# Optimization experiments

Hardware: AMD Instinct MI355X
Metric: run time of the kernel (lower is better)

The kernel has to match this reference:

```python
import jax, jax.numpy as jnp
import numpy as np
import math

BLOCK = 32
TAU = 0.1
INIT_SPARSITY = 0.1


def setup_inputs() -> dict:
    key = jax.random.key(0)
    k1, k2, k3, k4 = jax.random.split(key, 4)
    B, S, D_IN, D_OUT = 4, 2048, 4096, 4096
    x = jax.random.normal(k1, (B, S, D_IN), dtype=jnp.float32)
    # nn.Linear default init: uniform(-1/sqrt(in), 1/sqrt(in))
    bound = 1.0 / math.sqrt(D_IN)
    weight = jax.random.uniform(k2, (D_OUT, D_IN), minval=-bound, maxval=bound, dtype=jnp.float32)
    bias = jax.random.uniform(k3, (D_OUT,), minval=-bound, maxval=bound, dtype=jnp.float32)
    # scores init per _init_scores: randn*0.1 + logit(init_sparsity)
    target_logit = math.log(INIT_SPARSITY / (1.0 - INIT_SPARSITY))
    scores = jax.random.normal(k4, (D_OUT // BLOCK, D_IN // BLOCK), dtype=jnp.float32) * 0.1 + target_logit
    return {"x": x, "weight": weight, "bias": bias, "scores": scores}


def reference(x, weight, bias, scores):
    # block mask: sigmoid(scores) > tau, expanded 32x32 per block
    block_mask = (jax.nn.sigmoid(scores) > TAU).astype(weight.dtype)  # [O/32, I/32]
    full_mask = jnp.repeat(jnp.repeat(block_mask, BLOCK, axis=0), BLOCK, axis=1)  # [O, I]
    pruned_weight = weight * full_mask
    # F.linear: x @ W^T + b
    return jnp.einsum('bsi,oi->bso', x, pruned_weight) + bias
```

## Files before the change

### kernel.cpp

```cpp
#include <hip/hip_runtime.h>


#define BM 128
#define BN 128
#define BK 32

typedef __attribute__((ext_vector_type(8))) short bf16x8;
typedef __attribute__((ext_vector_type(4))) float f32x4;

__device__ __forceinline__ unsigned short f2bf(float f) {
    union { float f; unsigned u; } v; v.f = f;
    return (unsigned short)((v.u + 0x7FFFu + ((v.u >> 16) & 1u)) >> 16);
}

#define THRESH (-2.1972245773362196f)


__global__ void conv_x(const float* __restrict__ X, unsigned short* __restrict__ Xb) {
    const long i = ((long)blockIdx.x * 256 + threadIdx.x) * 8;
    const float4 a = *(const float4*)(X + i);
    const float4 b = *(const float4*)(X + i + 4);
    ushort4 p, q;
    p.x = f2bf(a.x); p.y = f2bf(a.y); p.z = f2bf(a.z); p.w = f2bf(a.w);
    q.x = f2bf(b.x); q.y = f2bf(b.y); q.z = f2bf(b.z); q.w = f2bf(b.w);
    *(ushort4*)(Xb + i) = p;
    *(ushort4*)(Xb + i + 4) = q;
}

__global__ void conv_w(const float* __restrict__ W, const float* __restrict__ scores,
                       unsigned short* __restrict__ Wb, int K, int KB) {
    const long i = ((long)blockIdx.x * 256 + threadIdx.x) * 8;
    const int n = (int)(i / K);
    const int k = (int)(i % K);
    const float msk = (scores[(n >> 5) * KB + (k >> 5)] > THRESH) ? 1.0f : 0.0f;
    const float4 a = *(const float4*)(W + i);
    const float4 b = *(const float4*)(W + i + 4);
    ushort4 p, q;
    p.x = f2bf(a.x * msk); p.y = f2bf(a.y * msk); p.z = f2bf(a.z * msk); p.w = f2bf(a.w * msk);
    q.x = f2bf(b.x * msk); q.y = f2bf(b.y * msk); q.z = f2bf(b.z * msk); q.w = f2bf(b.w * msk);
    *(ushort4*)(Wb + i) = p;
    *(ushort4*)(Wb + i + 4) = q;
}

__global__ void pack_mask(const float* __restrict__ scores, unsigned long long* __restrict__ mb,
                          int KB) {
    const int nb = blockIdx.x;
    const int l  = threadIdx.x;
    const unsigned long long b0 = __ballot(scores[nb * KB + l] > THRESH);
    const unsigned long long b1 = __ballot(scores[nb * KB + 64 + l] > THRESH);
    if (l == 0) { mb[nb * 2] = b0; mb[nb * 2 + 1] = b1; }
}


__device__ __forceinline__ unsigned long long rfl64(unsigned long long v) {
    unsigned lo = __builtin_amdgcn_readfirstlane((unsigned)v);
    unsigned hi = __builtin_amdgcn_readfirstlane((unsigned)(v >> 32));
    return ((unsigned long long)hi << 32) | lo;
}

#define GLL16(g, l) __builtin_amdgcn_global_load_lds( \
    (const __attribute__((address_space(1))) void*)(g), \
    (__attribute__((address_space(3))) void*)(l), 16, 0, 0)

__global__ __launch_bounds__(256)
void mpl_main(const unsigned short* __restrict__ Xb,
              const unsigned short* __restrict__ Wb,
              const float* __restrict__ bias,
              const unsigned long long* __restrict__ mb,
              float* __restrict__ out, int M, int N, int K)
{
    __shared__ unsigned short sA[BM * BK];
    __shared__ unsigned short sB[BN * BK];

    const int tid  = threadIdx.x;
    const int lane = tid & 63;
    const int wave = tid >> 6;
    const int m0   = blockIdx.y * BM;
    const int n0   = blockIdx.x * BN;
    const int wm   = (wave & 1) * 64;
    const int wn   = (wave >> 1) * 64;
    const int KB   = K >> 5;

    const int nbb  = n0 >> 5;
    const int mynb = nbb + (wn >> 5);
    const unsigned long long w0lo = rfl64(mb[mynb * 2]),       w0hi = rfl64(mb[mynb * 2 + 1]);
    const unsigned long long w1lo = rfl64(mb[(mynb + 1) * 2]), w1hi = rfl64(mb[(mynb + 1) * 2 + 1]);
    const unsigned long long anylo = rfl64(mb[nbb*2] | mb[nbb*2+2] | mb[nbb*2+4] | mb[nbb*2+6]);
    const unsigned long long anyhi = rfl64(mb[nbb*2+1] | mb[nbb*2+3] | mb[nbb*2+5] | mb[nbb*2+7]);

    f32x4 acc[4][4];
#pragma unroll
    for (int i = 0; i < 4; i++)
#pragma unroll
        for (int j = 0; j < 4; j++)
            acc[i][j] = (f32x4){0.f, 0.f, 0.f, 0.f};

    const int srow = tid >> 2;
    const int scol = (tid & 3) * 16;
    const char* gA0 = (const char*)Xb + (long)(m0 + srow) * K * 2 + scol;
    const char* gA1 = (const char*)Xb + (long)(m0 + srow + 64) * K * 2 + scol;
    const char* gB0 = (const char*)Wb + (long)(n0 + srow) * K * 2 + scol;
    const char* gB1 = (const char*)Wb + (long)(n0 + srow + 64) * K * 2 + scol;
    char* sAc = (char*)sA;
    char* sBc = (char*)sB;
    char* ldsA0 = sAc + wave * 1024;
    char* ldsA1 = sAc + wave * 1024 + 4096;
    char* ldsB0 = sBc + wave * 1024;
    char* ldsB1 = sBc + wave * 1024 + 4096;

    const int fr = lane & 15;
    const int kq = (lane >> 4) * 8;

    for (int kb = 0; kb < KB; kb++) {
        const bool any = (kb < 64) ? ((anylo >> kb) & 1ULL) : ((anyhi >> (kb - 64)) & 1ULL);
        if (!any) continue;

        const long ko = (long)kb * 64;
        GLL16(gA0 + ko, ldsA0);
        GLL16(gA1 + ko, ldsA1);
        GLL16(gB0 + ko, ldsB0);
        GLL16(gB1 + ko, ldsB1);
        __syncthreads();

        bf16x8 af[4];
#pragma unroll
        for (int mi = 0; mi < 4; mi++)
            af[mi] = *(const bf16x8*)&sA[(wm + mi * 16 + fr) * BK + kq];

        const bool b0 = (kb < 64) ? ((w0lo >> kb) & 1ULL) : ((w0hi >> (kb - 64)) & 1ULL);
        const bool b1 = (kb < 64) ? ((w1lo >> kb) & 1ULL) : ((w1hi >> (kb - 64)) & 1ULL);

        if (b0) {
            bf16x8 bf0 = *(const bf16x8*)&sB[(wn + 0 * 16 + fr) * BK + kq];
            bf16x8 bf1 = *(const bf16x8*)&sB[(wn + 1 * 16 + fr) * BK + kq];
#pragma unroll
            for (int mi = 0; mi < 4; mi++) {
                acc[mi][0] = __builtin_amdgcn_mfma_f32_16x16x32_bf16(af[mi], bf0, acc[mi][0], 0, 0, 0);
                acc[mi][1] = __builtin_amdgcn_mfma_f32_16x16x32_bf16(af[mi], bf1, acc[mi][1], 0, 0, 0);
            }
        }
        if (b1) {
            bf16x8 bf2 = *(const bf16x8*)&sB[(wn + 2 * 16 + fr) * BK + kq];
            bf16x8 bf3 = *(const bf16x8*)&sB[(wn + 3 * 16 + fr) * BK + kq];
#pragma unroll
            for (int mi = 0; mi < 4; mi++) {
                acc[mi][2] = __builtin_amdgcn_mfma_f32_16x16x32_bf16(af[mi], bf2, acc[mi][2], 0, 0, 0);
                acc[mi][3] = __builtin_amdgcn_mfma_f32_16x16x32_bf16(af[mi], bf3, acc[mi][3], 0, 0, 0);
            }
        }
        __syncthreads();
    }

    const int cn = lane & 15;
    const int rq = (lane >> 4) * 4;
#pragma unroll
    for (int ni = 0; ni < 4; ni++) {
        const int n = n0 + wn + ni * 16 + cn;
        const float b = bias[n];
#pragma unroll
        for (int mi = 0; mi < 4; mi++) {
#pragma unroll
            for (int r = 0; r < 4; r++) {
                const int m = m0 + wm + mi * 16 + rq + r;
                out[(long)m * N + n] = acc[mi][ni][r] + b;
            }
        }
    }
}


#define LDSS (BK + 8)
__global__ __launch_bounds__(256, 2)
void mpl_gemm_fb(const float* __restrict__ X, const float* __restrict__ W,
                 const float* __restrict__ bias, const float* __restrict__ scores,
                 float* __restrict__ out, int M, int N, int K)
{
    __shared__ unsigned short sA[BM * LDSS];
    __shared__ unsigned short sB[BN * LDSS];
    const int tid = threadIdx.x;
    const int m0 = blockIdx.y * BM, n0 = blockIdx.x * BN;
    const int wave = tid >> 6, lane = tid & 63;
    const int wm = (wave & 1) * 64, wn = (wave >> 1) * 64;
    const int kblocks = K >> 5;
    f32x4 acc[4][4];
#pragma unroll
    for (int i = 0; i < 4; i++)
#pragma unroll
        for (int j = 0; j < 4; j++) acc[i][j] = (f32x4){0.f,0.f,0.f,0.f};
    int srow[4], sc4[4], snb[4];
#pragma unroll
    for (int i = 0; i < 4; i++) {
        int f = tid + 256 * i;
        srow[i] = f >> 3; sc4[i] = f & 7; snb[i] = (n0 + srow[i]) >> 5;
    }
    for (int k0 = 0; k0 < K; k0 += BK) {
        const int kb = k0 >> 5;
#pragma unroll
        for (int i = 0; i < 4; i++) {
            const float4 v = *(const float4*)(X + (long)(m0 + srow[i]) * K + k0 + sc4[i] * 4);
            ushort4 p; p.x = f2bf(v.x); p.y = f2bf(v.y); p.z = f2bf(v.z); p.w = f2bf(v.w);
            *(ushort4*)&sA[srow[i] * LDSS + sc4[i] * 4] = p;
        }
#pragma unroll
        for (int i = 0; i < 4; i++) {
            const float msk = (scores[snb[i] * kblocks + kb] > THRESH) ? 1.0f : 0.0f;
            const float4 v = *(const float4*)(W + (long)(n0 + srow[i]) * K + k0 + sc4[i] * 4);
            ushort4 p; p.x = f2bf(v.x*msk); p.y = f2bf(v.y*msk); p.z = f2bf(v.z*msk); p.w = f2bf(v.w*msk);
            *(ushort4*)&sB[srow[i] * LDSS + sc4[i] * 4] = p;
        }
        __syncthreads();
        const int fr = lane & 15, kq = (lane >> 4) * 8;
        bf16x8 af[4], bfr[4];
#pragma unroll
        for (int mi = 0; mi < 4; mi++) af[mi] = *(const bf16x8*)&sA[(wm + mi*16 + fr) * LDSS + kq];
#pragma unroll
        for (int ni = 0; ni < 4; ni++) bfr[ni] = *(const bf16x8*)&sB[(wn + ni*16 + fr) * LDSS + kq];
#pragma unroll
        for (int mi = 0; mi < 4; mi++)
#pragma unroll
            for (int ni = 0; ni < 4; ni++)
                acc[mi][ni] = __builtin_amdgcn_mfma_f32_16x16x32_bf16(af[mi], bfr[ni], acc[mi][ni], 0,0,0);
        __syncthreads();
    }
    const int cn = lane & 15, rq = (lane >> 4) * 4;
#pragma unroll
    for (int ni = 0; ni < 4; ni++) {
        const int n = n0 + wn + ni * 16 + cn;
        const float b = bias[n];
#pragma unroll
        for (int mi = 0; mi < 4; mi++)
#pragma unroll
            for (int r = 0; r < 4; r++)
                out[(long)(m0 + wm + mi*16 + rq + r) * N + n] = acc[mi][ni][r] + b;
    }
}

extern "C" void kernel_launch(void* const* d_in, const int* in_sizes, int n_in,
                              void* d_out, int out_size, void* d_ws, size_t ws_size,
                              hipStream_t stream) {
    const float* X      = (const float*)d_in[0];
    const float* W      = (const float*)d_in[1];
    const float* bias   = (const float*)d_in[2];
    const float* scores = (const float*)d_in[3];
    float* out          = (float*)d_out;

    const int N = in_sizes[2];
    const int K = in_sizes[1] / N;
    const int M = in_sizes[0] / K;
    const int KB = K >> 5;
    const int NB = N >> 5;

    const size_t mk2 = (size_t)M * K * 2;
    const size_t nk2 = (size_t)N * K * 2;
    const size_t need = mk2 + nk2 + (size_t)NB * 16;

    if (ws_size >= need && KB == 128 && (M % 128) == 0 && (N % 128) == 0 && (K % 2048) == 0) {
        unsigned short* Xb = (unsigned short*)d_ws;
        unsigned short* Wb = (unsigned short*)((char*)d_ws + mk2);
        unsigned long long* mbits = (unsigned long long*)((char*)d_ws + mk2 + nk2);

        conv_x<<<(int)((long)M * K / 2048), 256, 0, stream>>>(X, Xb);
        conv_w<<<(int)((long)N * K / 2048), 256, 0, stream>>>(W, scores, Wb, K, KB);
        pack_mask<<<NB, 64, 0, stream>>>(scores, mbits, KB);

        dim3 grid(N / BN, M / BM);
        mpl_main<<<grid, dim3(256), 0, stream>>>(Xb, Wb, bias, mbits, out, M, N, K);
    } else {
        dim3 grid(N / BN, M / BM);
        mpl_gemm_fb<<<grid, dim3(256), 0, stream>>>(X, W, bias, scores, out, M, N, K);
    }
}
```

Measured before the change: 546.8 us.

## Double K tile to 64 with XOR-swizzled LDS and fuse prep kernels

Merges the three preprocessing kernels (X conversion, masked W conversion, mask bit packing) into one launch. It also doubles the main GEMM's K tile to 64 with an XOR-swizzled LDS layout to avoid bank conflicts. B loads are now skipped per 32-row block when that block's mask bits are zero. The larger tile halves the number of barriers per K and cuts launch overhead, at the cost of coarser skipping, since a 64-wide step loads if either 32-block is active.

New measurement: 477.6 us. 1.14x faster.

```diff
diff --git a/kernel.cpp b/kernel.cpp
--- a/kernel.cpp
+++ b/kernel.cpp
@@ -3,7 +3,7 @@
 
 #define BM 128
 #define BN 128
-#define BK 32
+#define BK 64
 
 typedef __attribute__((ext_vector_type(8))) short bf16x8;
 typedef __attribute__((ext_vector_type(4))) float f32x4;
@@ -15,40 +15,47 @@
 
 #define THRESH (-2.1972245773362196f)
 
-
-__global__ void conv_x(const float* __restrict__ X, unsigned short* __restrict__ Xb) {
-    const long i = ((long)blockIdx.x * 256 + threadIdx.x) * 8;
-    const float4 a = *(const float4*)(X + i);
-    const float4 b = *(const float4*)(X + i + 4);
-    ushort4 p, q;
-    p.x = f2bf(a.x); p.y = f2bf(a.y); p.z = f2bf(a.z); p.w = f2bf(a.w);
-    q.x = f2bf(b.x); q.y = f2bf(b.y); q.z = f2bf(b.z); q.w = f2bf(b.w);
-    *(ushort4*)(Xb + i) = p;
-    *(ushort4*)(Xb + i + 4) = q;
-}
-
-__global__ void conv_w(const float* __restrict__ W, const float* __restrict__ scores,
-                       unsigned short* __restrict__ Wb, int K, int KB) {
-    const long i = ((long)blockIdx.x * 256 + threadIdx.x) * 8;
-    const int n = (int)(i / K);
-    const int k = (int)(i % K);
-    const float msk = (scores[(n >> 5) * KB + (k >> 5)] > THRESH) ? 1.0f : 0.0f;
-    const float4 a = *(const float4*)(W + i);
-    const float4 b = *(const float4*)(W + i + 4);
-    ushort4 p, q;
-    p.x = f2bf(a.x * msk); p.y = f2bf(a.y * msk); p.z = f2bf(a.z * msk); p.w = f2bf(a.w * msk);
-    q.x = f2bf(b.x * msk); q.y = f2bf(b.y * msk); q.z = f2bf(b.z * msk); q.w = f2bf(b.w * msk);
-    *(ushort4*)(Wb + i) = p;
-    *(ushort4*)(Wb + i + 4) = q;
-}
-
-__global__ void pack_mask(const float* __restrict__ scores, unsigned long long* __restrict__ mb,
-                          int KB) {
-    const int nb = blockIdx.x;
-    const int l  = threadIdx.x;
-    const unsigned long long b0 = __ballot(scores[nb * KB + l] > THRESH);
-    const unsigned long long b1 = __ballot(scores[nb * KB + 64 + l] > THRESH);
-    if (l == 0) { mb[nb * 2] = b0; mb[nb * 2 + 1] = b1; }
+__global__ void prep(const float* __restrict__ X, const float* __restrict__ W,
+                     const float* __restrict__ scores,
+                     unsigned short* __restrict__ Xb, unsigned short* __restrict__ Wb,
+                     unsigned long long* __restrict__ mbits,
+                     int M, int N, int K) {
+    const int b   = blockIdx.x;
+    const int tid = threadIdx.x;
+    const int KBlk = K >> 5;
+
+    if (b < M + N) {
+        const float* src;
+        unsigned short* dst;
+        const bool isW = (b >= M);
+        const int n = isW ? (b - M) : 0;
+        if (isW) { src = W + (long)n * K; dst = Wb + (long)n * K; }
+        else     { src = X + (long)b * K; dst = Xb + (long)b * K; }
+        const float* srow = isW ? scores + (long)(n >> 5) * KBlk : nullptr;
+
+        for (int k = tid * 16; k < K; k += 4096) {
+            const float msk = isW ? ((srow[k >> 5] > THRESH) ? 1.0f : 0.0f) : 1.0f;
+            const float4 a = *(const float4*)(src + k);
+            const float4 c = *(const float4*)(src + k + 4);
+            const float4 e = *(const float4*)(src + k + 8);
+            const float4 g = *(const float4*)(src + k + 12);
+            ushort4 p, q, r, s;
+            p.x = f2bf(a.x * msk); p.y = f2bf(a.y * msk); p.z = f2bf(a.z * msk); p.w = f2bf(a.w * msk);
+            q.x = f2bf(c.x * msk); q.y = f2bf(c.y * msk); q.z = f2bf(c.z * msk); q.w = f2bf(c.w * msk);
+            r.x = f2bf(e.x * msk); r.y = f2bf(e.y * msk); r.z = f2bf(e.z * msk); r.w = f2bf(e.w * msk);
+            s.x = f2bf(g.x * msk); s.y = f2bf(g.y * msk); s.z = f2bf(g.z * msk); s.w = f2bf(g.w * msk);
+            *(ushort4*)(dst + k)      = p;
+            *(ushort4*)(dst + k + 4)  = q;
+            *(ushort4*)(dst + k + 8)  = r;
+            *(ushort4*)(dst + k + 12) = s;
+        }
+    } else {
+        const int nb = (b - (M + N)) * 4 + (tid >> 6);
+        const int l  = tid & 63;
+        const unsigned long long b0 = __ballot(scores[(long)nb * KBlk + l] > THRESH);
+        const unsigned long long b1 = __ballot(scores[(long)nb * KBlk + 64 + l] > THRESH);
+        if (l == 0) { mbits[nb * 2] = b0; mbits[nb * 2 + 1] = b1; }
+    }
 }
 
 
@@ -79,14 +86,15 @@
     const int n0   = blockIdx.x * BN;
     const int wm   = (wave & 1) * 64;
     const int wn   = (wave >> 1) * 64;
-    const int KB   = K >> 5;
-
-    const int nbb  = n0 >> 5;
-    const int mynb = nbb + (wn >> 5);
-    const unsigned long long w0lo = rfl64(mb[mynb * 2]),       w0hi = rfl64(mb[mynb * 2 + 1]);
-    const unsigned long long w1lo = rfl64(mb[(mynb + 1) * 2]), w1hi = rfl64(mb[(mynb + 1) * 2 + 1]);
-    const unsigned long long anylo = rfl64(mb[nbb*2] | mb[nbb*2+2] | mb[nbb*2+4] | mb[nbb*2+6]);
-    const unsigned long long anyhi = rfl64(mb[nbb*2+1] | mb[nbb*2+3] | mb[nbb*2+5] | mb[nbb*2+7]);
+    const long K2  = (long)K * 2;
+
+    const int nbb = n0 >> 5;
+    unsigned long long mlo[4], mhi[4];
+#pragma unroll
+    for (int i = 0; i < 4; i++) {
+        mlo[i] = rfl64(mb[(nbb + i) * 2]);
+        mhi[i] = rfl64(mb[(nbb + i) * 2 + 1]);
+    }
 
     f32x4 acc[4][4];
 #pragma unroll
@@ -95,60 +103,77 @@
         for (int j = 0; j < 4; j++)
             acc[i][j] = (f32x4){0.f, 0.f, 0.f, 0.f};
 
-    const int srow = tid >> 2;
-    const int scol = (tid & 3) * 16;
-    const char* gA0 = (const char*)Xb + (long)(m0 + srow) * K * 2 + scol;
-    const char* gA1 = (const char*)Xb + (long)(m0 + srow + 64) * K * 2 + scol;
-    const char* gB0 = (const char*)Wb + (long)(n0 + srow) * K * 2 + scol;
-    const char* gB1 = (const char*)Wb + (long)(n0 + srow + 64) * K * 2 + scol;
+    const int r8   = tid >> 3;
+    const int cswz = ((tid & 7) ^ ((tid >> 3) & 7)) * 16;
+    const char* gA = (const char*)Xb + (long)(m0 + r8) * K2 + cswz;
+    const char* gB = (const char*)Wb + (long)(n0 + r8) * K2 + cswz;
     char* sAc = (char*)sA;
     char* sBc = (char*)sB;
-    char* ldsA0 = sAc + wave * 1024;
-    char* ldsA1 = sAc + wave * 1024 + 4096;
-    char* ldsB0 = sBc + wave * 1024;
-    char* ldsB1 = sBc + wave * 1024 + 4096;
-
-    const int fr = lane & 15;
-    const int kq = (lane >> 4) * 8;
-
-    for (int kb = 0; kb < KB; kb++) {
-        const bool any = (kb < 64) ? ((anylo >> kb) & 1ULL) : ((anyhi >> (kb - 64)) & 1ULL);
-        if (!any) continue;
-
-        const long ko = (long)kb * 64;
-        GLL16(gA0 + ko, ldsA0);
-        GLL16(gA1 + ko, ldsA1);
-        GLL16(gB0 + ko, ldsB0);
-        GLL16(gB1 + ko, ldsB1);
-        __syncthreads();
-
-        bf16x8 af[4];
-#pragma unroll
-        for (int mi = 0; mi < 4; mi++)
-            af[mi] = *(const bf16x8*)&sA[(wm + mi * 16 + fr) * BK + kq];
-
-        const bool b0 = (kb < 64) ? ((w0lo >> kb) & 1ULL) : ((w0hi >> (kb - 64)) & 1ULL);
-        const bool b1 = (kb < 64) ? ((w1lo >> kb) & 1ULL) : ((w1hi >> (kb - 64)) & 1ULL);
-
-        if (b0) {
-            bf16x8 bf0 = *(const bf16x8*)&sB[(wn + 0 * 16 + fr) * BK + kq];
-            bf16x8 bf1 = *(const bf16x8*)&sB[(wn + 1 * 16 + fr) * BK + kq];
-#pragma unroll
-            for (int mi = 0; mi < 4; mi++) {
-                acc[mi][0] = __builtin_amdgcn_mfma_f32_16x16x32_bf16(af[mi], bf0, acc[mi][0], 0, 0, 0);
-                acc[mi][1] = __builtin_amdgcn_mfma_f32_16x16x32_bf16(af[mi], bf1, acc[mi][1], 0, 0, 0);
+    const int ldso = wave * 1024;
+
+    const int fr   = lane & 15;
+    const int cxor = lane & 7;
+    const int kqc  = lane >> 4;
+    const int rowA = wm + fr;
+    const int rowB = wn + fr;
+
+    int kb2 = 0;
+    for (int half = 0; half < 2; ++half) {
+        const unsigned long long w0 = half ? mhi[0] : mlo[0];
+        const unsigned long long w1 = half ? mhi[1] : mlo[1];
+        const unsigned long long w2 = half ? mhi[2] : mlo[2];
+        const unsigned long long w3 = half ? mhi[3] : mlo[3];
+        for (int q = 0; q < 32; ++q, ++kb2) {
+            const unsigned p0 = (unsigned)(w0 >> (2 * q)) & 3;
+            const unsigned p1 = (unsigned)(w1 >> (2 * q)) & 3;
+            const unsigned p2 = (unsigned)(w2 >> (2 * q)) & 3;
+            const unsigned p3 = (unsigned)(w3 >> (2 * q)) & 3;
+            if (!(p0 | p1 | p2 | p3)) continue;
+
+            const long ko = (long)kb2 * 128;
+#pragma unroll
+            for (int i = 0; i < 4; i++)
+                GLL16(gA + (long)i * 32 * K2 + ko, sAc + i * 4096 + ldso);
+            if (p0) GLL16(gB + 0L * 32 * K2 + ko, sBc + 0 * 4096 + ldso);
+            if (p1) GLL16(gB + 1L * 32 * K2 + ko, sBc + 1 * 4096 + ldso);
+            if (p2) GLL16(gB + 2L * 32 * K2 + ko, sBc + 2 * 4096 + ldso);
+            if (p3) GLL16(gB + 3L * 32 * K2 + ko, sBc + 3 * 4096 + ldso);
+            __syncthreads();
+
+            const unsigned plo = (wave >> 1) ? p2 : p0;
+            const unsigned phi = (wave >> 1) ? p3 : p1;
+
+#pragma unroll
+            for (int kbl = 0; kbl < 2; ++kbl) {
+                if (!(((plo | phi) >> kbl) & 1)) continue;
+                const int boff = ((kqc | (kbl << 2)) ^ cxor) * 16;
+
+                bf16x8 af[4];
+#pragma unroll
+                for (int mi = 0; mi < 4; mi++)
+                    af[mi] = *(const bf16x8*)(sAc + (rowA + mi * 16) * 128 + boff);
+
+                if ((plo >> kbl) & 1) {
+                    const bf16x8 bf0 = *(const bf16x8*)(sBc + (rowB + 0)  * 128 + boff);
+                    const bf16x8 bf1 = *(const bf16x8*)(sBc + (rowB + 16) * 128 + boff);
+#pragma unroll
+                    for (int mi = 0; mi < 4; mi++) {
+                        acc[mi][0] = __builtin_amdgcn_mfma_f32_16x16x32_bf16(af[mi], bf0, acc[mi][0], 0, 0, 0);
+                        acc[mi][1] = __builtin_amdgcn_mfma_f32_16x16x32_bf16(af[mi], bf1, acc[mi][1], 0, 0, 0);
+                    }
+                }
+                if ((phi >> kbl) & 1) {
+                    const bf16x8 bf2 = *(const bf16x8*)(sBc + (rowB + 32) * 128 + boff);
+                    const bf16x8 bf3 = *(const bf16x8*)(sBc + (rowB + 48) * 128 + boff);
+#pragma unroll
+                    for (int mi = 0; mi < 4; mi++) {
+                        acc[mi][2] = __builtin_amdgcn_mfma_f32_16x16x32_bf16(af[mi], bf2, acc[mi][2], 0, 0, 0);
+                        acc[mi][3] = __builtin_amdgcn_mfma_f32_16x16x32_bf16(af[mi], bf3, acc[mi][3], 0, 0, 0);
+                    }
+                }
             }
-        }
-        if (b1) {
-            bf16x8 bf2 = *(const bf16x8*)&sB[(wn + 2 * 16 + fr) * BK + kq];
-            bf16x8 bf3 = *(const bf16x8*)&sB[(wn + 3 * 16 + fr) * BK + kq];
-#pragma unroll
-            for (int mi = 0; mi < 4; mi++) {
-                acc[mi][2] = __builtin_amdgcn_mfma_f32_16x16x32_bf16(af[mi], bf2, acc[mi][2], 0, 0, 0);
-                acc[mi][3] = __builtin_amdgcn_mfma_f32_16x16x32_bf16(af[mi], bf3, acc[mi][3], 0, 0, 0);
-            }
-        }
-        __syncthreads();
+            __syncthreads();
+        }
     }
 
     const int cn = lane & 15;
@@ -169,7 +194,8 @@
 }
 
 
-#define LDSS (BK + 8)
+#define FBK 32
+#define LDSS (FBK + 8)
 __global__ __launch_bounds__(256, 2)
 void mpl_gemm_fb(const float* __restrict__ X, const float* __restrict__ W,
                  const float* __restrict__ bias, const float* __restrict__ scores,
@@ -193,7 +219,7 @@
         int f = tid + 256 * i;
         srow[i] = f >> 3; sc4[i] = f & 7; snb[i] = (n0 + srow[i]) >> 5;
     }
-    for (int k0 = 0; k0 < K; k0 += BK) {
+    for (int k0 = 0; k0 < K; k0 += FBK) {
         const int kb = k0 >> 5;
 #pragma unroll
         for (int i = 0; i < 4; i++) {
@@ -254,14 +280,13 @@
     const size_t nk2 = (size_t)N * K * 2;
     const size_t need = mk2 + nk2 + (size_t)NB * 16;
 
-    if (ws_size >= need && KB == 128 && (M % 128) == 0 && (N % 128) == 0 && (K % 2048) == 0) {
+    if (ws_size >= need && KB == 128 && (M % 128) == 0 && (N % 128) == 0 &&
+        (K % 4096) == 0 && (NB % 4) == 0) {
         unsigned short* Xb = (unsigned short*)d_ws;
         unsigned short* Wb = (unsigned short*)((char*)d_ws + mk2);
         unsigned long long* mbits = (unsigned long long*)((char*)d_ws + mk2 + nk2);
 
-        conv_x<<<(int)((long)M * K / 2048), 256, 0, stream>>>(X, Xb);
-        conv_w<<<(int)((long)N * K / 2048), 256, 0, stream>>>(W, scores, Wb, K, KB);
-        pack_mask<<<NB, 64, 0, stream>>>(scores, mbits, KB);
+        prep<<<M + N + NB / 4, 256, 0, stream>>>(X, W, scores, Xb, Wb, mbits, M, N, K);
 
         dim3 grid(N / BN, M / BM);
         mpl_main<<<grid, dim3(256), 0, stream>>>(Xb, Wb, bias, mbits, out, M, N, K);
```
